# Kernel optimization log

Hardware: AMD Instinct MI355X
Metric: run time of the kernel (lower is better)

The kernel has to match this reference:

```python
import jax, jax.numpy as jnp
import numpy as np


def setup_inputs() -> dict:
    key = jax.random.key(0)
    ks = jax.random.split(key, 4)
    B, T, D, U = 64, 2048, 256, 256
    x = jax.random.normal(ks[0], (B, T, D), dtype=jnp.float32)
    s = 1.0 / np.sqrt(D)
    kz = jax.random.normal(ks[1], (D, U), dtype=jnp.float32) * s
    kr = jax.random.normal(ks[2], (D, U), dtype=jnp.float32) * s
    kh = jax.random.normal(ks[3], (D, U), dtype=jnp.float32) * s
    return {
        'x': x, 'kz': kz, 'kr': kr, 'kh': kh,
        'mz': jnp.ones((U,), jnp.float32), 'mr': jnp.ones((U,), jnp.float32),
        'bz': jnp.zeros((U,), jnp.float32), 'br': jnp.zeros((U,), jnp.float32),
        'bh': jnp.zeros((U,), jnp.float32),
    }


def reference(x, kz, kr, kh, mz, mr, bz, br, bh):
    # Precompute the three input projections for all timesteps (batched GEMMs),
    # then scan the purely elementwise recurrence over time.
    xz = jnp.einsum('btd,du->btu', x, kz) + bz  # [B,T,U]
    xr = jnp.einsum('btd,du->btu', x, kr) + br
    xh = jnp.einsum('btd,du->btu', x, kh) + bh
    B, T, U = xz.shape
    h0 = jnp.zeros((B, U), x.dtype)

    def step(h, inp):
        xz_t, xr_t, xh_t = inp
        r = jnp.tanh(xr_t + h * mr) + 1.0
        z = jax.nn.sigmoid(xz_t + h * mz)
        hh = jnp.tanh(xh_t + r * h)
        out = (1.0 - z) * hh + z * h
        return out, out

    # scan over time axis: move T to leading axis
    xs = (jnp.swapaxes(xz, 0, 1), jnp.swapaxes(xr, 0, 1), jnp.swapaxes(xh, 0, 1))
    _, ys = jax.lax.scan(step, h0, xs)
    return jnp.swapaxes(ys, 0, 1)  # [B,T,U]
```

## Files before the change

kernel.cpp:

```cpp
#include <hip/hip_runtime.h>
#include <hip/hip_bf16.h>

#define BB 64
#define TT 2048
#define DD 256
#define UU 256
#define MM (BB*TT)
#define NN (3*UU)
#define PLANE ((size_t)BB*TT*UU)

typedef _Float16 half8 __attribute__((ext_vector_type(8)));
typedef _Float16 half4 __attribute__((ext_vector_type(4)));
typedef float floatx4 __attribute__((ext_vector_type(4)));

__device__ inline float fexp2(float x){
#if __has_builtin(__builtin_amdgcn_exp2f)
  return __builtin_amdgcn_exp2f(x);
#else
  return exp2f(x);
#endif
}
__device__ inline float frcp(float x){
#if __has_builtin(__builtin_amdgcn_rcpf)
  return __builtin_amdgcn_rcpf(x);
#else
  return 1.0f/x;
#endif
}
__device__ inline float ftanh(float a){
  const float TWO_L2E = 2.8853900817779268f;
  return 1.0f - 2.0f*frcp(fexp2(TWO_L2E*a) + 1.0f);
}
__device__ inline float fsigmoid(float a){
  const float L2E = 1.4426950408889634f;
  return frcp(1.0f + fexp2(-L2E*a));
}

__global__ __launch_bounds__(256) void prep_kernel(const float* __restrict__ kz,
                                                   const float* __restrict__ kr,
                                                   const float* __restrict__ kh,
                                                   _Float16* __restrict__ K16T){
  int o = blockIdx.x*256 + threadIdx.x;
  int n = o >> 8;
  int k = o & 255;
  int p = n >> 8;
  int u = n & 255;
  const float* w = (p==0) ? kz : ((p==1) ? kr : kh);
  K16T[o] = (_Float16)w[k*UU + u];
}

#define BM 128
#define BN 128
#define BK 32
#define LDA 40

__global__ __launch_bounds__(256) void gemm_kernel(const float* __restrict__ X,
                                                   const _Float16* __restrict__ K16T,
                                                   const float* __restrict__ bz,
                                                   const float* __restrict__ br,
                                                   const float* __restrict__ bh,
                                                   _Float16* __restrict__ P){
  __shared__ __align__(16) _Float16 As[BM*LDA];
  __shared__ __align__(16) _Float16 Bs[BN*BK];
  const int tid = threadIdx.x;

  const int l   = blockIdx.y*6 + blockIdx.x;
  const int xcd = l & 7;
  const int idx = l >> 3;
  const int pnl = idx / 6;
  const int by  = xcd*128 + pnl;
  const int bx  = idx - pnl*6;
  const int rowBase = by*BM;
  const int nBase   = bx*BN;

  const int wave = tid >> 6, lane = tid & 63;
  const int wm = wave & 1, wn = wave >> 1;
  const int lrow = lane & 15, lkq = lane >> 4;

  floatx4 acc[4][4] = {};

  const int arow = tid >> 1;
  const int acol = (tid & 1) * 16;
  const float* aptr = X + (size_t)(rowBase + arow)*DD + acol;
  _Float16* asdst = &As[arow*LDA + acol];

  for (int k0 = 0; k0 < DD; k0 += BK) {
    __syncthreads();
    floatx4 a0 = *(const floatx4*)(aptr + k0);
    floatx4 a1 = *(const floatx4*)(aptr + k0 + 4);
    floatx4 a2 = *(const floatx4*)(aptr + k0 + 8);
    floatx4 a3 = *(const floatx4*)(aptr + k0 + 12);
    #pragma unroll
    for (int i = 0; i < 2; i++) {
      int c = i*256 + tid;
      const _Float16* g = K16T + (size_t)(nBase + (c>>2))*DD + k0 + (c&3)*8;
      __builtin_amdgcn_global_load_lds(
          (const __attribute__((address_space(1))) void*)g,
          (__attribute__((address_space(3))) void*)(Bs + c*8),
          16, 0, 0);
    }
    half8 pk0, pk1;
    #pragma unroll
    for (int q = 0; q < 4; q++){
      pk0[q]   = (_Float16)a0[q];
      pk0[4+q] = (_Float16)a1[q];
      pk1[q]   = (_Float16)a2[q];
      pk1[4+q] = (_Float16)a3[q];
    }
    *(half8*)asdst       = pk0;
    *(half8*)(asdst + 8) = pk1;
    __syncthreads();
    half8 af[4], bf[4];
    #pragma unroll
    for (int i = 0; i < 4; i++)
      af[i] = *(const half8*)&As[(wm*64 + i*16 + lrow)*LDA + lkq*8];
    #pragma unroll
    for (int j = 0; j < 4; j++)
      bf[j] = *(const half8*)&Bs[(wn*64 + j*16 + lrow)*BK + lkq*8];
    #pragma unroll
    for (int i = 0; i < 4; i++)
      #pragma unroll
      for (int j = 0; j < 4; j++)
        acc[i][j] = __builtin_amdgcn_mfma_f32_16x16x32_f16(af[i], bf[j], acc[i][j], 0, 0, 0);
  }

  const int p = bx >> 1;
  const int ub = (bx & 1) * 128;
  const float* bias = (p==0) ? bz : ((p==1) ? br : bh);
  _Float16* Pp = P + (size_t)p * PLANE;
  const int bidx = rowBase >> 11;
  const int t0 = (rowBase & 2047) + wm*64 + lkq*4;
  #pragma unroll
  for (int j = 0; j < 4; j++){
    int col = ub + wn*64 + j*16 + lrow;
    float bv = bias[col];
    _Float16* rowp = Pp + (size_t)(bidx*UU + col)*TT + t0;
    #pragma unroll
    for (int i = 0; i < 4; i++){
      half4 v;
      #pragma unroll
      for (int r = 0; r < 4; r++)
        v[r] = (_Float16)(acc[i][j][r] + bv);
      *(half4*)(rowp + i*16) = v;
    }
  }
}

#define PF 16
#define NBUF 4
__global__ __launch_bounds__(64) void scan_kernel(const _Float16* __restrict__ P,
                                                  const float* __restrict__ mz,
                                                  const float* __restrict__ mr,
                                                  float* __restrict__ out){
  const int ci = blockIdx.x*64 + threadIdx.x;
  const int b = ci >> 8;
  const int u = ci & 255;
  const half8* pz = (const half8*)(P + (size_t)ci*TT);
  const half8* pr = (const half8*)(P + PLANE + (size_t)ci*TT);
  const half8* ph = (const half8*)(P + 2*PLANE + (size_t)ci*TT);
  float* po = out + (size_t)b*(TT*UU) + u;
  const float vmz = mz[u], vmr = mr[u];
  float h = 0.0f;

  half8 qz[NBUF][2], qr[NBUF][2], qh[NBUF][2];

#define LOADC(buf, c) do { \
    qz[buf][0] = pz[(c)*2];   qz[buf][1] = pz[(c)*2+1]; \
    qr[buf][0] = pr[(c)*2];   qr[buf][1] = pr[(c)*2+1]; \
    qh[buf][0] = ph[(c)*2];   qh[buf][1] = ph[(c)*2+1]; \
  } while(0)

#define PROC(buf, c) do { \
    _Pragma("unroll") \
    for (int i = 0; i < PF; i++){ \
      float xz = (float)qz[buf][i>>3][i&7]; \
      float xr = (float)qr[buf][i>>3][i&7]; \
      float xh = (float)qh[buf][i>>3][i&7]; \
      float r  = ftanh(xr + h*vmr) + 1.0f; \
      float z  = fsigmoid(xz + h*vmz); \
      float hh = ftanh(xh + r*h); \
      h = (1.0f - z)*hh + z*h; \
      po[(size_t)((c)*PF + i)*UU] = h; \
    } \
    if ((c) + NBUF < NC) LOADC(buf, (c) + NBUF); \
  } while(0)

  const int NC = TT/PF;
  LOADC(0, 0); LOADC(1, 1); LOADC(2, 2); LOADC(3, 3);
  for (int c = 0; c < NC; c += NBUF){
    PROC(0, c);
    PROC(1, c+1);
    PROC(2, c+2);
    PROC(3, c+3);
  }
#undef LOADC
#undef PROC
}

extern "C" void kernel_launch(void* const* d_in, const int* in_sizes, int n_in,
                              void* d_out, int out_size, void* d_ws, size_t ws_size,
                              hipStream_t stream) {
  (void)in_sizes; (void)n_in; (void)out_size; (void)ws_size;
  const float* x  = (const float*)d_in[0];
  const float* kz = (const float*)d_in[1];
  const float* kr = (const float*)d_in[2];
  const float* kh = (const float*)d_in[3];
  const float* mz = (const float*)d_in[4];
  const float* mr = (const float*)d_in[5];
  const float* bz = (const float*)d_in[6];
  const float* br = (const float*)d_in[7];
  const float* bh = (const float*)d_in[8];
  float* out = (float*)d_out;

  _Float16* K16T = (_Float16*)d_ws;
  _Float16* P    = (_Float16*)((char*)d_ws + 393216);

  hipLaunchKernelGGL(prep_kernel, dim3(NN*DD/256), dim3(256), 0, stream, kz, kr, kh, K16T);
  hipLaunchKernelGGL(gemm_kernel, dim3(NN/BN, MM/BM), dim3(256), 0, stream,
                     x, K16T, bz, br, bh, P);
  hipLaunchKernelGGL(scan_kernel, dim3(256), dim3(64), 0, stream, P, mz, mr, out);
}
```

Baseline: 473.5 us.

## Rearrange GEMM LDS layout into k-chunk planes and stage epilogue through LDS

The A and B tiles in shared memory now use a k-chunk-major layout (one 8-element chunk per row per plane), which removes the padded row stride and should reduce bank conflicts for the MFMA fragment reads. The B global-to-LDS loads are remapped to match. The epilogue no longer scatters 8-byte half4 stores along the transposed time axis; it transposes each 64-column half through LDS and writes contiguous 64-byte runs per output row, which should improve store coalescing into the time-major P buffer. In exchange the epilogue adds two block-wide barriers per half and leaves half the waves idle during each staging pass.

```diff
diff --git a/kernel.cpp b/kernel.cpp
--- a/kernel.cpp
+++ b/kernel.cpp
@@ -52,7 +52,9 @@
 #define BM 128
 #define BN 128
 #define BK 32
-#define LDA 40
+#define AS_OFF 0
+#define BS_OFF 4096
+#define CT_LDT 136
 
 __global__ __launch_bounds__(256) void gemm_kernel(const float* __restrict__ X,
                                                    const _Float16* __restrict__ K16T,
@@ -60,8 +62,7 @@
                                                    const float* __restrict__ br,
                                                    const float* __restrict__ bh,
                                                    _Float16* __restrict__ P){
-  __shared__ __align__(16) _Float16 As[BM*LDA];
-  __shared__ __align__(16) _Float16 Bs[BN*BK];
+  __shared__ __align__(16) _Float16 smem[8704];
   const int tid = threadIdx.x;
 
   const int l   = blockIdx.y*6 + blockIdx.x;
@@ -79,10 +80,13 @@
 
   floatx4 acc[4][4] = {};
 
-  const int arow = tid >> 1;
-  const int acol = (tid & 1) * 16;
-  const float* aptr = X + (size_t)(rowBase + arow)*DD + acol;
-  _Float16* asdst = &As[arow*LDA + acol];
+  const int arow = tid & 127;
+  const int asel = tid >> 7;
+  const float* aptr = X + (size_t)(rowBase + arow)*DD + asel*16;
+  _Float16* aw0 = smem + AS_OFF + ((asel*2 + 0)*128 + arow)*8;
+  _Float16* aw1 = smem + AS_OFF + ((asel*2 + 1)*128 + arow)*8;
+
+  const _Float16* bsrc = K16T + (size_t)(nBase + (tid & 127))*DD + (tid >> 7)*8;
 
   for (int k0 = 0; k0 < DD; k0 += BK) {
     __syncthreads();
@@ -90,15 +94,14 @@
     floatx4 a1 = *(const floatx4*)(aptr + k0 + 4);
     floatx4 a2 = *(const floatx4*)(aptr + k0 + 8);
     floatx4 a3 = *(const floatx4*)(aptr + k0 + 12);
-    #pragma unroll
-    for (int i = 0; i < 2; i++) {
-      int c = i*256 + tid;
-      const _Float16* g = K16T + (size_t)(nBase + (c>>2))*DD + k0 + (c&3)*8;
-      __builtin_amdgcn_global_load_lds(
-          (const __attribute__((address_space(1))) void*)g,
-          (__attribute__((address_space(3))) void*)(Bs + c*8),
-          16, 0, 0);
-    }
+    __builtin_amdgcn_global_load_lds(
+        (const __attribute__((address_space(1))) void*)(bsrc + k0),
+        (__attribute__((address_space(3))) void*)(smem + BS_OFF + tid*8),
+        16, 0, 0);
+    __builtin_amdgcn_global_load_lds(
+        (const __attribute__((address_space(1))) void*)(bsrc + k0 + 16),
+        (__attribute__((address_space(3))) void*)(smem + BS_OFF + (tid + 256)*8),
+        16, 0, 0);
     half8 pk0, pk1;
     #pragma unroll
     for (int q = 0; q < 4; q++){
@@ -107,16 +110,16 @@
       pk1[q]   = (_Float16)a2[q];
       pk1[4+q] = (_Float16)a3[q];
     }
-    *(half8*)asdst       = pk0;
-    *(half8*)(asdst + 8) = pk1;
+    *(half8*)aw0 = pk0;
+    *(half8*)aw1 = pk1;
     __syncthreads();
     half8 af[4], bf[4];
     #pragma unroll
     for (int i = 0; i < 4; i++)
-      af[i] = *(const half8*)&As[(wm*64 + i*16 + lrow)*LDA + lkq*8];
+      af[i] = *(const half8*)&smem[AS_OFF + (lkq*128 + wm*64 + i*16 + lrow)*8];
     #pragma unroll
     for (int j = 0; j < 4; j++)
-      bf[j] = *(const half8*)&Bs[(wn*64 + j*16 + lrow)*BK + lkq*8];
+      bf[j] = *(const half8*)&smem[BS_OFF + (lkq*128 + wn*64 + j*16 + lrow)*8];
     #pragma unroll
     for (int i = 0; i < 4; i++)
       #pragma unroll
@@ -128,21 +131,34 @@
   const int ub = (bx & 1) * 128;
   const float* bias = (p==0) ? bz : ((p==1) ? br : bh);
   _Float16* Pp = P + (size_t)p * PLANE;
-  const int bidx = rowBase >> 11;
-  const int t0 = (rowBase & 2047) + wm*64 + lkq*4;
+  const int bidx  = rowBase >> 11;
+  const int trow0 = rowBase & 2047;
+  const int u_r = tid >> 2, tc = tid & 3;
+
   #pragma unroll
-  for (int j = 0; j < 4; j++){
-    int col = ub + wn*64 + j*16 + lrow;
-    float bv = bias[col];
-    _Float16* rowp = Pp + (size_t)(bidx*UU + col)*TT + t0;
-    #pragma unroll
-    for (int i = 0; i < 4; i++){
-      half4 v;
+  for (int h = 0; h < 2; h++){
+    __syncthreads();
+    if (wn == h){
       #pragma unroll
-      for (int r = 0; r < 4; r++)
-        v[r] = (_Float16)(acc[i][j][r] + bv);
-      *(half4*)(rowp + i*16) = v;
+      for (int j = 0; j < 4; j++){
+        const int u_l = j*16 + lrow;
+        const float bv = bias[ub + h*64 + u_l];
+        #pragma unroll
+        for (int i = 0; i < 4; i++){
+          half4 v;
+          #pragma unroll
+          for (int r = 0; r < 4; r++)
+            v[r] = (_Float16)(acc[i][j][r] + bv);
+          *(half4*)&smem[u_l*CT_LDT + wm*64 + i*16 + lkq*4] = v;
+        }
+      }
     }
+    __syncthreads();
+    _Float16* dst = Pp + (size_t)(bidx*UU + ub + h*64 + u_r)*TT + trow0 + tc*32;
+    const _Float16* srcp = smem + u_r*CT_LDT + tc*32;
+    #pragma unroll
+    for (int q = 0; q < 4; q++)
+      *(half8*)(dst + q*8) = *(const half8*)(srcp + q*8);
   }
 }
 
```

Result: slower. 524.0 us (+10.7%).
